# Kernel optimization log

Measured on AMD Instinct MI355X. Metric: run time of the kernel, lower is better.

The kernel has to match this reference:

```python
import jax, jax.numpy as jnp
import numpy as np

# Static problem dims (all graphs equal-sized so adaptive pool = uniform bins)
B = 64          # graphs
N = 2048        # nodes per graph
E = 16          # node_emb_dim
H_OUT, W_OUT = 32, 4   # AdaptiveAvgPool2d output -> pooled_dim = 128
COND = 64       # cond_emb_dim
HID = 512       # mlp_h_dim
BN_EPS = 1e-5


def _lin_init(key, out_d, in_d):
    kw, kb = jax.random.split(key)
    lim = 1.0 / np.sqrt(in_d)
    W = jax.random.uniform(kw, (out_d, in_d), jnp.float32, -lim, lim)
    b = jax.random.uniform(kb, (out_d,), jnp.float32, -lim, lim)
    return W, b


def setup_inputs() -> dict:
    key = jax.random.key(0)
    ks = jax.random.split(key, 6)
    Ntot = B * N
    x = jax.random.normal(ks[0], (Ntot, E), jnp.float32)
    batch = jnp.repeat(jnp.arange(B, dtype=jnp.int32), N)  # sorted segment ids
    cond = jax.random.normal(ks[1], (Ntot, COND), jnp.float32)
    mlp_in = COND + H_OUT * W_OUT  # 192
    W1, b1 = _lin_init(ks[2], HID, mlp_in)
    W2, b2 = _lin_init(ks[3], HID, HID)
    W3, b3 = _lin_init(ks[4], 3, HID)
    g1 = jnp.ones((HID,), jnp.float32); be1 = jnp.zeros((HID,), jnp.float32)
    g2 = jnp.ones((HID,), jnp.float32); be2 = jnp.zeros((HID,), jnp.float32)
    return {"x": x, "batch": batch, "conditioner_z_ref": cond,
            "W1": W1, "b1": b1, "g1": g1, "be1": be1,
            "W2": W2, "b2": b2, "g2": g2, "be2": be2,
            "W3": W3, "b3": b3}


def _bn_gelu(h, g, be):
    # BatchNorm1d in training mode: biased batch stats over the node axis
    m = h.mean(axis=0)
    v = h.var(axis=0)
    h = g * (h - m) * jax.lax.rsqrt(v + BN_EPS) + be
    return jax.nn.gelu(h, approximate=False)


def reference(x, batch, conditioner_z_ref, W1, b1, g1, be1, W2, b2, g2, be2, W3, b3):
    # Per-graph adaptive avg pool: since N % H_OUT == 0 and E % W_OUT == 0,
    # AdaptiveAvgPool2d is exactly mean over uniform (N/H_OUT, E/W_OUT) bins.
    xb = x.reshape(B, H_OUT, N // H_OUT, W_OUT, E // W_OUT)
    batch_pooled = xb.mean(axis=(2, 4)).reshape(B, H_OUT * W_OUT)  # [B, 128]
    pooled_per_node = batch_pooled[batch]                           # gather to [Ntot, 128]
    h = jnp.concatenate([conditioner_z_ref, pooled_per_node], axis=1)  # [Ntot, 192]
    h = _bn_gelu(h @ W1.T + b1, g1, be1)
    h = _bn_gelu(h @ W2.T + b2, g2, be2)
    return h @ W3.T + b3  # [Ntot, 3] predicted coords
```

## Files before the change

kernel.cpp:

```cpp
#include <hip/hip_runtime.h>
#include <hip/hip_bf16.h>
#include <math.h>
#include <stdint.h>

#define B_GRAPHS 64
#define N_NODES  2048
#define E_DIM    16
#define M_TOT    (B_GRAPHS * N_NODES)
#define K_COND   64
#define MLP_IN   192
#define HID      512
#define POOLD    128
#define BN_EPS   1e-5f

typedef __attribute__((ext_vector_type(8))) short bfrag8;
typedef __attribute__((ext_vector_type(4))) float facc4;

__device__ __forceinline__ unsigned short f2b(float f) {
    unsigned int x = __builtin_bit_cast(unsigned int, f);
    unsigned int r = x + 0x7fffu + ((x >> 16) & 1u);
    return (unsigned short)(r >> 16);
}
__device__ __forceinline__ float b2f(unsigned short u) {
    unsigned int x = ((unsigned int)u) << 16;
    return __builtin_bit_cast(float, x);
}

__device__ __forceinline__ float gelu_fast(float y) {
    float x  = y * 0.70710678118654752440f;
    float ax = fabsf(x);
    float t  = __builtin_amdgcn_rcpf(fmaf(0.3275911f, ax, 1.0f));
    float p  = fmaf(1.061405429f, t, -1.453152027f);
    p = fmaf(p, t, 1.421413741f);
    p = fmaf(p, t, -0.284496736f);
    p = fmaf(p, t, 0.254829592f);
    p = p * t;
    float e = __expf(-x * x);
    float erfax = fmaf(-p, e, 1.0f);
    float erfx  = copysignf(erfax, x);
    return 0.5f * y * (1.0f + erfx);
}

#define GLOAD_LDS16(g, l)                                                        \
    __builtin_amdgcn_global_load_lds(                                            \
        (const __attribute__((address_space(1))) unsigned int*)(const void*)(g), \
        (__attribute__((address_space(3))) unsigned int*)(void*)(l), 16, 0, 0)

__global__ __launch_bounds__(512) void prep_kernel(const float* __restrict__ x,
                                                   const float* __restrict__ W1,
                                                   const float* __restrict__ b1,
                                                   float* __restrict__ gbias) {
    __shared__ float pl[POOLD];
    int g = blockIdx.x, t = threadIdx.x;
    if (t < 128) {
        int h = t >> 2, w = t & 3;
        const float* base = x + (size_t)g * N_NODES * E_DIM + (size_t)h * 64 * E_DIM + w * 4;
        float s = 0.f;
        #pragma unroll 4
        for (int r = 0; r < 64; ++r) {
            float4 v = *reinterpret_cast<const float4*>(base + (size_t)r * E_DIM);
            s += v.x + v.y + v.z + v.w;
        }
        pl[h * 4 + w] = s * (1.0f / 256.0f);
    }
    __syncthreads();
    const float* wr_ = W1 + (size_t)t * MLP_IN + K_COND;
    float s = b1[t];
    #pragma unroll 4
    for (int k = 0; k < POOLD; ++k) s = fmaf(pl[k], wr_[k], s);
    gbias[g * HID + t] = s;
}

__global__ __launch_bounds__(256) void cvt_kernel(const float* __restrict__ s,
                                                  unsigned short* __restrict__ d) {
    size_t i = ((size_t)blockIdx.x * 256 + threadIdx.x) * 8;
    float4 v0 = *reinterpret_cast<const float4*>(s + i);
    float4 v1 = *reinterpret_cast<const float4*>(s + i + 4);
    unsigned short t[8] = {f2b(v0.x), f2b(v0.y), f2b(v0.z), f2b(v0.w),
                           f2b(v1.x), f2b(v1.y), f2b(v1.z), f2b(v1.w)};
    *reinterpret_cast<bfrag8*>(d + i) = *reinterpret_cast<bfrag8*>(t);
}

__device__ __forceinline__ bfrag8 load_f32x8_as_bf16(const float* p) {
    float4 v0 = *reinterpret_cast<const float4*>(p);
    float4 v1 = *reinterpret_cast<const float4*>(p + 4);
    unsigned short t[8] = {f2b(v0.x), f2b(v0.y), f2b(v0.z), f2b(v0.w),
                           f2b(v1.x), f2b(v1.y), f2b(v1.z), f2b(v1.w)};
    return *reinterpret_cast<bfrag8*>(t);
}

__global__ __launch_bounds__(256) void gemm1_kernel(const float* __restrict__ A,
                                                    const float* __restrict__ W,
                                                    const int* __restrict__ batch,
                                                    const float* __restrict__ gbias,
                                                    float* __restrict__ sums,
                                                    unsigned short* __restrict__ C) {
    __shared__ float sArr[128], qArr[128];
    const int t = threadIdx.x;
    const int r0 = blockIdx.x * 128, c0 = blockIdx.y * 128;
    const int l = t & 63, w = t >> 6;
    const int wr = w >> 1, wc = w & 1;
    const int ln = l & 15, kg = l >> 4;
    if (t < 128) { sArr[t] = 0.f; qArr[t] = 0.f; }
    __syncthreads();

    facc4 acc[4][4];
    const facc4 z = {0.f, 0.f, 0.f, 0.f};
    #pragma unroll
    for (int a = 0; a < 4; ++a)
        #pragma unroll
        for (int b = 0; b < 4; ++b) acc[a][b] = z;

    #pragma unroll
    for (int ks = 0; ks < 2; ++ks) {
        bfrag8 af[4], bf[4];
        #pragma unroll
        for (int a = 0; a < 4; ++a)
            af[a] = load_f32x8_as_bf16(A + (size_t)(r0 + wr * 64 + a * 16 + ln) * K_COND + ks * 32 + kg * 8);
        #pragma unroll
        for (int b = 0; b < 4; ++b)
            bf[b] = load_f32x8_as_bf16(W + (size_t)(c0 + wc * 64 + b * 16 + ln) * MLP_IN + ks * 32 + kg * 8);
        #pragma unroll
        for (int a = 0; a < 4; ++a)
            #pragma unroll
            for (int b = 0; b < 4; ++b)
                acc[a][b] = __builtin_amdgcn_mfma_f32_16x16x32_bf16(af[a], bf[b], acc[a][b], 0, 0, 0);
    }

    float cs[4] = {0.f, 0.f, 0.f, 0.f}, cq[4] = {0.f, 0.f, 0.f, 0.f};
    #pragma unroll
    for (int a = 0; a < 4; ++a) {
        #pragma unroll
        for (int i = 0; i < 4; ++i) {
            int row = r0 + wr * 64 + a * 16 + kg * 4 + i;
            const float* gb = gbias + (size_t)batch[row] * HID;
            size_t rbase = (size_t)row * HID + c0 + wc * 64 + ln;
            #pragma unroll
            for (int b = 0; b < 4; ++b) {
                float v = acc[a][b][i] + gb[c0 + wc * 64 + b * 16 + ln];
                C[rbase + b * 16] = f2b(v);
                cs[b] += v; cq[b] = fmaf(v, v, cq[b]);
            }
        }
    }
    #pragma unroll
    for (int b = 0; b < 4; ++b) {
        cs[b] += __shfl_xor(cs[b], 16, 64); cq[b] += __shfl_xor(cq[b], 16, 64);
        cs[b] += __shfl_xor(cs[b], 32, 64); cq[b] += __shfl_xor(cq[b], 32, 64);
    }
    if (kg == 0) {
        #pragma unroll
        for (int b = 0; b < 4; ++b) {
            int cl = wc * 64 + b * 16 + ln;
            atomicAdd(&sArr[cl], cs[b]); atomicAdd(&qArr[cl], cq[b]);
        }
    }
    __syncthreads();
    if (t < 128) {
        atomicAdd(&sums[c0 + t], sArr[t]);
        atomicAdd(&sums[HID + c0 + t], qArr[t]);
    }
}

__global__ __launch_bounds__(512) void gemm2_kernel(const unsigned short* __restrict__ A,
                                                    const unsigned short* __restrict__ Bm,
                                                    const float* __restrict__ sums1,
                                                    const float* __restrict__ g1,
                                                    const float* __restrict__ be1,
                                                    const float* __restrict__ bias,
                                                    float* __restrict__ sums,
                                                    unsigned short* __restrict__ C) {
    __shared__ unsigned short As[2][128 * 32];
    __shared__ unsigned short Bs[2][256 * 32];
    __shared__ float lss[2 * HID];
    __shared__ float sArr[256], qArr[256];
    const int t = threadIdx.x;
    const int r0 = blockIdx.x * 128, c0 = blockIdx.y * 256;
    const int l = t & 63, w = t >> 6;
    const int wr = w >> 2, wc = w & 3;
    const int ln = l & 15, kg = l >> 4;
    const int arow = t >> 2, aslot = t & 3;
    const int rr = l >> 2, sp = l & 3;
    const int bss = sp ^ ((rr >> 1) & 3);

    {
        float mean = sums1[t] * (1.0f / M_TOT);
        float var  = sums1[HID + t] * (1.0f / M_TOT) - mean * mean;
        float sc   = g1[t] * rsqrtf(var + BN_EPS);
        lss[t] = sc;
        lss[HID + t] = be1[t] - mean * sc;
    }
    if (t < 256) { sArr[t] = 0.f; qArr[t] = 0.f; }

    facc4 acc[4][4];
    const facc4 z = {0.f, 0.f, 0.f, 0.f};
    #pragma unroll
    for (int a = 0; a < 4; ++a)
        #pragma unroll
        for (int b = 0; b < 4; ++b) acc[a][b] = z;

    const unsigned short* aptr = A + (size_t)(r0 + arow) * HID + aslot * 8;
    const int awslot = aslot ^ ((arow >> 1) & 3);

    __syncthreads();

    {
        bfrag8 va = *reinterpret_cast<const bfrag8*>(aptr);
        unsigned short tmp[8];
        #pragma unroll
        for (int j = 0; j < 8; ++j) {
            int col = aslot * 8 + j;
            float xv = b2f((unsigned short)va[j]);
            tmp[j] = f2b(gelu_fast(fmaf(xv, lss[col], lss[HID + col])));
        }
        *reinterpret_cast<bfrag8*>(&As[0][arow * 32 + awslot * 8]) = *reinterpret_cast<bfrag8*>(tmp);
        #pragma unroll
        for (int c = 0; c < 2; ++c) {
            int chunk = w * 2 + c;
            const unsigned short* gb = Bm + (size_t)(c0 + chunk * 16 + rr) * HID + bss * 8;
            GLOAD_LDS16(gb, &Bs[0][chunk * 512]);
        }
    }
    __syncthreads();

    for (int step = 0; step < 16; ++step) {
        const int cur = step & 1;
        bfrag8 af[4], bf[4];
        #pragma unroll
        for (int a = 0; a < 4; ++a) {
            int RA = wr * 64 + a * 16 + ln;
            af[a] = *reinterpret_cast<const bfrag8*>(&As[cur][RA * 32 + (kg ^ ((RA >> 1) & 3)) * 8]);
        }
        #pragma unroll
        for (int b = 0; b < 4; ++b) {
            int RB = wc * 64 + b * 16 + ln;
            bf[b] = *reinterpret_cast<const bfrag8*>(&Bs[cur][RB * 32 + (kg ^ ((RB >> 1) & 3)) * 8]);
        }
        bfrag8 va;
        const bool pf = step < 15;
        if (pf) {
            const int kk = step * 32 + 32;
            va = *reinterpret_cast<const bfrag8*>(aptr + kk);
            #pragma unroll
            for (int c = 0; c < 2; ++c) {
                int chunk = w * 2 + c;
                const unsigned short* gb = Bm + (size_t)(c0 + chunk * 16 + rr) * HID + kk + bss * 8;
                GLOAD_LDS16(gb, &Bs[cur ^ 1][chunk * 512]);
            }
        }
        #pragma unroll
        for (int a = 0; a < 4; ++a)
            #pragma unroll
            for (int b = 0; b < 4; ++b)
                acc[a][b] = __builtin_amdgcn_mfma_f32_16x16x32_bf16(af[a], bf[b], acc[a][b], 0, 0, 0);
        if (pf) {
            const int kk = step * 32 + 32;
            unsigned short tmp[8];
            #pragma unroll
            for (int j = 0; j < 8; ++j) {
                int col = kk + aslot * 8 + j;
                float xv = b2f((unsigned short)va[j]);
                tmp[j] = f2b(gelu_fast(fmaf(xv, lss[col], lss[HID + col])));
            }
            *reinterpret_cast<bfrag8*>(&As[cur ^ 1][arow * 32 + awslot * 8]) = *reinterpret_cast<bfrag8*>(tmp);
        }
        __syncthreads();
    }

    float bb[4];
    #pragma unroll
    for (int b = 0; b < 4; ++b) bb[b] = bias[c0 + wc * 64 + b * 16 + ln];
    float cs[4] = {0.f, 0.f, 0.f, 0.f}, cq[4] = {0.f, 0.f, 0.f, 0.f};
    #pragma unroll
    for (int a = 0; a < 4; ++a) {
        #pragma unroll
        for (int i = 0; i < 4; ++i) {
            size_t rbase = (size_t)(r0 + wr * 64 + a * 16 + kg * 4 + i) * HID + c0 + wc * 64 + ln;
            #pragma unroll
            for (int b = 0; b < 4; ++b) {
                float v = acc[a][b][i] + bb[b];
                C[rbase + b * 16] = f2b(v);
                cs[b] += v; cq[b] = fmaf(v, v, cq[b]);
            }
        }
    }
    #pragma unroll
    for (int b = 0; b < 4; ++b) {
        cs[b] += __shfl_xor(cs[b], 16, 64); cq[b] += __shfl_xor(cq[b], 16, 64);
        cs[b] += __shfl_xor(cs[b], 32, 64); cq[b] += __shfl_xor(cq[b], 32, 64);
    }
    if (kg == 0) {
        #pragma unroll
        for (int b = 0; b < 4; ++b) {
            int cl = wc * 64 + b * 16 + ln;
            atomicAdd(&sArr[cl], cs[b]); atomicAdd(&qArr[cl], cq[b]);
        }
    }
    __syncthreads();
    if (t < 256) {
        atomicAdd(&sums[c0 + t], sArr[t]);
        atomicAdd(&sums[HID + c0 + t], qArr[t]);
    }
}

__global__ void finalize_kernel(const float* __restrict__ sums, const float* __restrict__ g,
                                const float* __restrict__ be, float* __restrict__ ss) {
    int n = threadIdx.x;
    float mean = sums[n] * (1.0f / M_TOT);
    float var = sums[HID + n] * (1.0f / M_TOT) - mean * mean;
    float sc = g[n] * rsqrtf(var + BN_EPS);
    ss[n] = sc;
    ss[HID + n] = be[n] - mean * sc;
}

__global__ __launch_bounds__(256) void g3_kernel(const unsigned short* __restrict__ H2,
                                                 const float* __restrict__ ss2,
                                                 const float* __restrict__ W3,
                                                 const float* __restrict__ b3,
                                                 float* __restrict__ out) {
    __shared__ float lss[2 * HID];
    __shared__ float lw3[3 * HID];
    int t = threadIdx.x;
    for (int i = t; i < 2 * HID; i += 256) lss[i] = ss2[i];
    for (int i = t; i < 3 * HID; i += 256) lw3[i] = W3[i];
    __syncthreads();
    int l = t & 63, w = t >> 6;
    int rsub = l >> 3, lk = l & 7;
    int row = blockIdx.x * 32 + w * 8 + rsub;
    const unsigned short* p = H2 + (size_t)row * HID;
    float o0 = 0.f, o1 = 0.f, o2 = 0.f;
    #pragma unroll
    for (int it = 0; it < 8; ++it) {
        int k = it * 64 + lk * 8;
        bfrag8 v = *reinterpret_cast<const bfrag8*>(p + k);
        #pragma unroll
        for (int j = 0; j < 8; ++j) {
            float x = b2f((unsigned short)v[j]);
            float y = fmaf(x, lss[k + j], lss[HID + k + j]);
            y = gelu_fast(y);
            o0 = fmaf(y, lw3[k + j], o0);
            o1 = fmaf(y, lw3[HID + k + j], o1);
            o2 = fmaf(y, lw3[2 * HID + k + j], o2);
        }
    }
    #pragma unroll
    for (int m = 1; m < 8; m <<= 1) {
        o0 += __shfl_xor(o0, m, 64);
        o1 += __shfl_xor(o1, m, 64);
        o2 += __shfl_xor(o2, m, 64);
    }
    if (lk == 0) {
        out[(size_t)row * 3 + 0] = o0 + b3[0];
        out[(size_t)row * 3 + 1] = o1 + b3[1];
        out[(size_t)row * 3 + 2] = o2 + b3[2];
    }
}

extern "C" void kernel_launch(void* const* d_in, const int* in_sizes, int n_in,
                              void* d_out, int out_size, void* d_ws, size_t ws_size,
                              hipStream_t stream) {
    const float* x     = (const float*)d_in[0];
    const int*   batch = (const int*)d_in[1];
    const float* cond  = (const float*)d_in[2];
    const float* W1    = (const float*)d_in[3];
    const float* b1    = (const float*)d_in[4];
    const float* g1    = (const float*)d_in[5];
    const float* be1   = (const float*)d_in[6];
    const float* W2    = (const float*)d_in[7];
    const float* b2    = (const float*)d_in[8];
    const float* g2    = (const float*)d_in[9];
    const float* be2   = (const float*)d_in[10];
    const float* W3    = (const float*)d_in[11];
    const float* b3    = (const float*)d_in[12];

    const size_t H_BYTES = (size_t)M_TOT * HID * 2;
    if (ws_size < 2 * H_BYTES) return;
    char* ws = (char*)d_ws;
    unsigned short* H1 = (unsigned short*)ws;
    unsigned short* H2 = (unsigned short*)(ws + H_BYTES);

    float* outf   = (float*)d_out;
    float* gbias  = outf;
    float* sums1  = gbias + B_GRAPHS * HID;
    float* sums2  = sums1 + 2 * HID;
    unsigned short* W2bf = (unsigned short*)(sums2 + 2 * HID);
    float* ss2 = (float*)ws;

    hipMemsetAsync(sums1, 0, 2 * 2 * HID * sizeof(float), stream);

    prep_kernel<<<B_GRAPHS, 512, 0, stream>>>(x, W1, b1, gbias);
    cvt_kernel<<<(HID * HID / 8) / 256, 256, 0, stream>>>(W2, W2bf);

    gemm1_kernel<<<dim3(M_TOT / 128, HID / 128), 256, 0, stream>>>(
        cond, W1, batch, gbias, sums1, H1);

    gemm2_kernel<<<dim3(M_TOT / 128, HID / 256), 512, 0, stream>>>(
        H1, W2bf, sums1, g1, be1, b2, sums2, H2);

    finalize_kernel<<<1, HID, 0, stream>>>(sums2, g2, be2, ss2);

    g3_kernel<<<M_TOT / 32, 256, 0, stream>>>(H2, ss2, W3, b3, outf);
}
```

Measured before the change: 335.4 us.

## Widen gemm2 tile to full 512 columns and prefetch A two steps ahead

gemm2 now computes a 128x512 output tile per block instead of 128x256, so each block covers all hidden columns. The BN1+GELU transform of the A operand is therefore done once per row rather than twice, and H1 is read once. The A global load is also issued two K-steps ahead to hide latency. The cost is twice as many accumulators per thread (128 floats) and a doubled B shared buffer, which pressures registers and occupancy; launch_bounds(512,2) may force spills.

```diff
diff --git a/kernel.cpp b/kernel.cpp
--- a/kernel.cpp
+++ b/kernel.cpp
@@ -162,24 +162,25 @@
     }
 }
 
-__global__ __launch_bounds__(512) void gemm2_kernel(const unsigned short* __restrict__ A,
-                                                    const unsigned short* __restrict__ Bm,
-                                                    const float* __restrict__ sums1,
-                                                    const float* __restrict__ g1,
-                                                    const float* __restrict__ be1,
-                                                    const float* __restrict__ bias,
-                                                    float* __restrict__ sums,
-                                                    unsigned short* __restrict__ C) {
+__global__ __launch_bounds__(512, 2) void gemm2_kernel(const unsigned short* __restrict__ A,
+                                                       const unsigned short* __restrict__ Bm,
+                                                       const float* __restrict__ sums1,
+                                                       const float* __restrict__ g1,
+                                                       const float* __restrict__ be1,
+                                                       const float* __restrict__ bias,
+                                                       float* __restrict__ sums,
+                                                       unsigned short* __restrict__ C) {
     __shared__ unsigned short As[2][128 * 32];
-    __shared__ unsigned short Bs[2][256 * 32];
+    __shared__ unsigned short Bs[2][512 * 32];
     __shared__ float lss[2 * HID];
-    __shared__ float sArr[256], qArr[256];
+    __shared__ float sArr[HID], qArr[HID];
     const int t = threadIdx.x;
-    const int r0 = blockIdx.x * 128, c0 = blockIdx.y * 256;
+    const int r0 = blockIdx.x * 128;
     const int l = t & 63, w = t >> 6;
     const int wr = w >> 2, wc = w & 3;
     const int ln = l & 15, kg = l >> 4;
     const int arow = t >> 2, aslot = t & 3;
+    const int awslot = aslot ^ ((arow >> 1) & 3);
     const int rr = l >> 2, sp = l & 3;
     const int bss = sp ^ ((rr >> 1) & 3);
 
@@ -190,94 +191,97 @@
         lss[t] = sc;
         lss[HID + t] = be1[t] - mean * sc;
     }
-    if (t < 256) { sArr[t] = 0.f; qArr[t] = 0.f; }
-
-    facc4 acc[4][4];
+    sArr[t] = 0.f; qArr[t] = 0.f;
+
+    facc4 acc[4][8];
     const facc4 z = {0.f, 0.f, 0.f, 0.f};
     #pragma unroll
     for (int a = 0; a < 4; ++a)
         #pragma unroll
-        for (int b = 0; b < 4; ++b) acc[a][b] = z;
+        for (int b = 0; b < 8; ++b) acc[a][b] = z;
 
     const unsigned short* aptr = A + (size_t)(r0 + arow) * HID + aslot * 8;
-    const int awslot = aslot ^ ((arow >> 1) & 3);
-
-    __syncthreads();
-
+    __syncthreads();
+
+    bfrag8 va_pending;
     {
-        bfrag8 va = *reinterpret_cast<const bfrag8*>(aptr);
+        bfrag8 va0 = *reinterpret_cast<const bfrag8*>(aptr);
         unsigned short tmp[8];
         #pragma unroll
         for (int j = 0; j < 8; ++j) {
             int col = aslot * 8 + j;
-            float xv = b2f((unsigned short)va[j]);
+            float xv = b2f((unsigned short)va0[j]);
             tmp[j] = f2b(gelu_fast(fmaf(xv, lss[col], lss[HID + col])));
         }
         *reinterpret_cast<bfrag8*>(&As[0][arow * 32 + awslot * 8]) = *reinterpret_cast<bfrag8*>(tmp);
         #pragma unroll
-        for (int c = 0; c < 2; ++c) {
-            int chunk = w * 2 + c;
-            const unsigned short* gb = Bm + (size_t)(c0 + chunk * 16 + rr) * HID + bss * 8;
+        for (int c = 0; c < 4; ++c) {
+            int chunk = w * 4 + c;
+            const unsigned short* gb = Bm + (size_t)(chunk * 16 + rr) * HID + bss * 8;
             GLOAD_LDS16(gb, &Bs[0][chunk * 512]);
         }
-    }
-    __syncthreads();
-
+        va_pending = *reinterpret_cast<const bfrag8*>(aptr + 32);
+    }
+    __syncthreads();
+
+    #pragma unroll 2
     for (int step = 0; step < 16; ++step) {
-        const int cur = step & 1;
-        bfrag8 af[4], bf[4];
+        const int cur = step & 1, nxt = cur ^ 1;
+        bfrag8 af[4], bf[8];
         #pragma unroll
         for (int a = 0; a < 4; ++a) {
             int RA = wr * 64 + a * 16 + ln;
             af[a] = *reinterpret_cast<const bfrag8*>(&As[cur][RA * 32 + (kg ^ ((RA >> 1) & 3)) * 8]);
         }
         #pragma unroll
-        for (int b = 0; b < 4; ++b) {
-            int RB = wc * 64 + b * 16 + ln;
+        for (int b = 0; b < 8; ++b) {
+            int RB = wc * 128 + b * 16 + ln;
             bf[b] = *reinterpret_cast<const bfrag8*>(&Bs[cur][RB * 32 + (kg ^ ((RB >> 1) & 3)) * 8]);
         }
-        bfrag8 va;
-        const bool pf = step < 15;
-        if (pf) {
-            const int kk = step * 32 + 32;
-            va = *reinterpret_cast<const bfrag8*>(aptr + kk);
-            #pragma unroll
-            for (int c = 0; c < 2; ++c) {
-                int chunk = w * 2 + c;
-                const unsigned short* gb = Bm + (size_t)(c0 + chunk * 16 + rr) * HID + kk + bss * 8;
-                GLOAD_LDS16(gb, &Bs[cur ^ 1][chunk * 512]);
+        if (step < 15) {
+            const int kk = (step + 1) * 32;
+            #pragma unroll
+            for (int c = 0; c < 4; ++c) {
+                int chunk = w * 4 + c;
+                const unsigned short* gb = Bm + (size_t)(chunk * 16 + rr) * HID + kk + bss * 8;
+                GLOAD_LDS16(gb, &Bs[nxt][chunk * 512]);
             }
         }
+        bfrag8 va_future;
+        if (step < 14) va_future = *reinterpret_cast<const bfrag8*>(aptr + (step + 2) * 32);
         #pragma unroll
         for (int a = 0; a < 4; ++a)
             #pragma unroll
-            for (int b = 0; b < 4; ++b)
+            for (int b = 0; b < 8; ++b)
                 acc[a][b] = __builtin_amdgcn_mfma_f32_16x16x32_bf16(af[a], bf[b], acc[a][b], 0, 0, 0);
-        if (pf) {
-            const int kk = step * 32 + 32;
+        if (step < 15) {
+            const int kk = (step + 1) * 32;
             unsigned short tmp[8];
             #pragma unroll
             for (int j = 0; j < 8; ++j) {
                 int col = kk + aslot * 8 + j;
-                float xv = b2f((unsigned short)va[j]);
+                float xv = b2f((unsigned short)va_pending[j]);
                 tmp[j] = f2b(gelu_fast(fmaf(xv, lss[col], lss[HID + col])));
             }
-            *reinterpret_cast<bfrag8*>(&As[cur ^ 1][arow * 32 + awslot * 8]) = *reinterpret_cast<bfrag8*>(tmp);
-        }
+            *reinterpret_cast<bfrag8*>(&As[nxt][arow * 32 + awslot * 8]) = *reinterpret_cast<bfrag8*>(tmp);
+        }
+        va_pending = va_future;
         __syncthreads();
     }
 
-    float bb[4];
-    #pragma unroll
-    for (int b = 0; b < 4; ++b) bb[b] = bias[c0 + wc * 64 + b * 16 + ln];
-    float cs[4] = {0.f, 0.f, 0.f, 0.f}, cq[4] = {0.f, 0.f, 0.f, 0.f};
+    float bb[8];
+    #pragma unroll
+    for (int b = 0; b < 8; ++b) bb[b] = bias[wc * 128 + b * 16 + ln];
+    float cs[8], cq[8];
+    #pragma unroll
+    for (int b = 0; b < 8; ++b) { cs[b] = 0.f; cq[b] = 0.f; }
     #pragma unroll
     for (int a = 0; a < 4; ++a) {
         #pragma unroll
         for (int i = 0; i < 4; ++i) {
-            size_t rbase = (size_t)(r0 + wr * 64 + a * 16 + kg * 4 + i) * HID + c0 + wc * 64 + ln;
-            #pragma unroll
-            for (int b = 0; b < 4; ++b) {
+            size_t rbase = (size_t)(r0 + wr * 64 + a * 16 + kg * 4 + i) * HID + wc * 128 + ln;
+            #pragma unroll
+            for (int b = 0; b < 8; ++b) {
                 float v = acc[a][b][i] + bb[b];
                 C[rbase + b * 16] = f2b(v);
                 cs[b] += v; cq[b] = fmaf(v, v, cq[b]);
@@ -285,22 +289,20 @@
         }
     }
     #pragma unroll
-    for (int b = 0; b < 4; ++b) {
+    for (int b = 0; b < 8; ++b) {
         cs[b] += __shfl_xor(cs[b], 16, 64); cq[b] += __shfl_xor(cq[b], 16, 64);
         cs[b] += __shfl_xor(cs[b], 32, 64); cq[b] += __shfl_xor(cq[b], 32, 64);
     }
     if (kg == 0) {
         #pragma unroll
-        for (int b = 0; b < 4; ++b) {
-            int cl = wc * 64 + b * 16 + ln;
+        for (int b = 0; b < 8; ++b) {
+            int cl = wc * 128 + b * 16 + ln;
             atomicAdd(&sArr[cl], cs[b]); atomicAdd(&qArr[cl], cq[b]);
         }
     }
     __syncthreads();
-    if (t < 256) {
-        atomicAdd(&sums[c0 + t], sArr[t]);
-        atomicAdd(&sums[HID + c0 + t], qArr[t]);
-    }
+    atomicAdd(&sums[t], sArr[t]);
+    atomicAdd(&sums[HID + t], qArr[t]);
 }
 
 __global__ void finalize_kernel(const float* __restrict__ sums, const float* __restrict__ g,
@@ -394,7 +396,7 @@
     gemm1_kernel<<<dim3(M_TOT / 128, HID / 128), 256, 0, stream>>>(
         cond, W1, batch, gbias, sums1, H1);
 
-    gemm2_kernel<<<dim3(M_TOT / 128, HID / 256), 512, 0, stream>>>(
+    gemm2_kernel<<<dim3(M_TOT / 128, 1), 512, 0, stream>>>(
         H1, W2bf, sums1, g1, be1, b2, sums2, H2);
 
     finalize_kernel<<<1, HID, 0, stream>>>(sums2, g2, be2, ss2);
```

Measured after the change: 313.3 us. 6.6% less time.
